# Kernel optimization log

Measured on AMD Instinct MI355X. Metric: run time of the kernel, lower is better.

## Reference

```python
import jax, jax.numpy as jnp
import numpy as np

NUM_HEADS = 8
WIN = (7, 7)


def _relative_position_index(wh, ww):
    # Same construction as the torch module (numpy, static).
    coords = np.stack(np.meshgrid(np.arange(wh), np.arange(ww), indexing='ij'))  # (2, wh, ww)
    flat = coords.reshape(2, -1)                                                 # (2, L)
    rel = flat[:, :, None] - flat[:, None, :]                                    # (2, L, L)
    rel = rel.transpose(1, 2, 0).astype(np.int64)                                # (L, L, 2)
    rel[:, :, 0] += wh - 1
    rel[:, :, 1] += ww - 1
    rel[:, :, 0] *= 2 * ww - 1
    return rel.sum(-1)  # (L, L), values in [0, (2wh-1)*(2ww-1))


def setup_inputs() -> dict:
    key = jax.random.key(0)
    k0, k1, k2, k3, k4 = jax.random.split(key, 5)
    B, C = 2048, 256
    wh, ww = WIN
    L = wh * ww
    nW = 64
    q = jax.random.normal(k0, (B, C, wh, ww), dtype=jnp.float32)
    k = jax.random.normal(k1, (B, C, wh, ww), dtype=jnp.float32)
    v = jax.random.normal(k2, (B, C, wh, ww), dtype=jnp.float32)
    # Swin-style shift mask: 0 where attend, -100 where blocked
    keep = jax.random.uniform(k3, (nW, L, L)) < 0.9
    mask = jnp.where(keep, 0.0, -100.0).astype(jnp.float32)
    n_bias = (2 * wh - 1) * (2 * ww - 1)  # 169
    rel_bias_table = 0.02 * jax.random.normal(k4, (n_bias, NUM_HEADS), dtype=jnp.float32)
    rel_pos_index = jnp.asarray(_relative_position_index(wh, ww), dtype=jnp.int32)
    return {"q": q, "k": k, "v": v, "mask": mask,
            "rel_bias_table": rel_bias_table, "rel_pos_index": rel_pos_index}


def reference(q, k, v, mask, rel_bias_table, rel_pos_index):
    b, c, wh, ww = q.shape
    L = wh * ww
    H = NUM_HEADS
    d_k = c // H
    scale = d_k ** -0.5
    qh = q.reshape(b, H, d_k, L)
    kh = k.reshape(b, H, d_k, L)
    # NOTE: the original torch code reassigns v = k.reshape(...) — values come from k.
    vh = kh
    attn = jnp.einsum('bhct,bhcs->bhts', qh, kh) * scale  # (b, H, L, L)
    bias = rel_bias_table[rel_pos_index.reshape(-1)].reshape(L, L, H)
    attn = attn + jnp.transpose(bias, (2, 0, 1))[None]    # (1, H, L, L)
    nW = mask.shape[0]
    attn = attn.reshape(b // nW, nW, H, L, L) + mask[None, :, None]
    attn = attn.reshape(b, H, L, L)
    attn = jax.nn.softmax(attn, axis=-1)
    score = jnp.einsum('bhts,bhcs->bhct', attn, vh).reshape(b, c, wh, ww)
    return (score, attn)
```

## Files before the change

### kernel.cpp

```cpp
#include <hip/hip_runtime.h>
#include <hip/hip_bf16.h>
#include <math.h>


#define LW 49
#define NH 8

typedef short s16x8 __attribute__((ext_vector_type(8)));
typedef float f32x4 __attribute__((ext_vector_type(4)));

union Frag { s16x8 v; unsigned short u[8]; };

__device__ __forceinline__ unsigned short f2bf(float x) {
    return __builtin_bit_cast(unsigned short, __float2bfloat16(x));
}
__device__ __forceinline__ float bf2f(unsigned short h) {
    return __uint_as_float(((unsigned)h) << 16);
}
__device__ __forceinline__ void split8(const float* xf, Frag& hi, Frag& lo) {
    #pragma unroll
    for (int j = 0; j < 8; j++) {
        const unsigned short hb = f2bf(xf[j]);
        hi.u[j] = hb;
        lo.u[j] = f2bf(xf[j] - bf2f(hb));
    }
}

__device__ __forceinline__ void lds_barrier() {
    asm volatile("s_waitcnt lgkmcnt(0)" ::: "memory");
    __builtin_amdgcn_s_barrier();
    asm volatile("" ::: "memory");
    __builtin_amdgcn_sched_barrier(0);
}

#define MFMA16(A, B, C) __builtin_amdgcn_mfma_f32_16x16x32_bf16((A), (B), (C), 0, 0, 0)

__global__ __launch_bounds__(256) void prep_frag_kernel(
    const float* __restrict__ mask, const float* __restrict__ table,
    const int* __restrict__ idx,
    float* __restrict__ biasF, float* __restrict__ maskF)
{
    const int i = blockIdx.x * 256 + threadIdx.x;
    const int NBF = 8 * 4096;
    const int NMF = 64 * 4096;
    if (i < NBF) {
        const int h = i >> 12, rem = i & 4095;
        const int gi = rem >> 8, lane = (rem >> 2) & 63, r = rem & 3;
        const int mt = gi >> 2, nt = gi & 3;
        const int t = mt * 16 + (lane >> 4) * 4 + r;
        const int s = nt * 16 + (lane & 15);
        biasF[i] = (t < LW && s < LW) ? table[idx[t * LW + s] * NH + h] : 0.f;
    } else if (i < NBF + NMF) {
        const int j = i - NBF;
        const int w2 = j >> 12, rem = j & 4095;
        const int gi = rem >> 8, lane = (rem >> 2) & 63, r = rem & 3;
        const int mt = gi >> 2, nt = gi & 3;
        const int t = mt * 16 + (lane >> 4) * 4 + r;
        const int s = nt * 16 + (lane & 15);
        maskF[j] = (t < LW && s < LW) ? mask[w2 * (LW * LW) + t * LW + s] : 0.f;
    }
}

__global__ __launch_bounds__(128, 4) void wa_mfma_kernel(
    const float* __restrict__ q, const float* __restrict__ k,
    const float* __restrict__ biasF, const float* __restrict__ maskF,
    float* __restrict__ score_out, float* __restrict__ attn_out)
{
    __shared__ __align__(16) unsigned short sB[6272];

    const int wv   = __builtin_amdgcn_readfirstlane((int)(threadIdx.x >> 6));
    const int bh   = blockIdx.x;
    const int h    = bh & 7;
    const int w    = (bh >> 3) & 63;
    const int lane = threadIdx.x & 63;
    const int l15  = lane & 15;
    const int g4   = lane >> 4;

    const float* qp = q + (size_t)bh * (32 * LW);
    const float* kp = k + (size_t)bh * (32 * LW);

    float k1raw[2][8], qraw[2][8], k2raw[2][8];
    #pragma unroll
    for (int ki = 0; ki < 2; ki++) {
        const int s  = (wv * 2 + ki) * 16 + l15;
        const int sc = s < LW ? s : (LW - 1);
        #pragma unroll
        for (int j = 0; j < 8; j++) k1raw[ki][j] = kp[(g4 * 8 + j) * LW + sc];
    }
    #pragma unroll
    for (int mi = 0; mi < 2; mi++) {
        const int t  = (wv * 2 + mi) * 16 + l15;
        const int tc = t < LW ? t : (LW - 1);
        #pragma unroll
        for (int j = 0; j < 8; j++) qraw[mi][j] = qp[(g4 * 8 + j) * LW + tc];
    }
    {
        const int c = wv * 16 + l15;
        #pragma unroll
        for (int ks = 0; ks < 2; ks++)
            #pragma unroll
            for (int j = 0; j < 8; j++) {
                const int s  = ks * 32 + g4 * 8 + j;
                const int sc = s < LW ? s : (LW - 1);
                k2raw[ks][j] = kp[c * LW + sc];
            }
    }

    #pragma unroll
    for (int ki = 0; ki < 2; ki++) {
        const int nt = wv * 2 + ki;
        Frag Kh, Kl;
        split8(k1raw[ki], Kh, Kl);
        *(s16x8*)&sB[nt * 512 + lane * 8]        = Kh.v;
        *(s16x8*)&sB[2048 + nt * 512 + lane * 8] = Kl.v;
    }

    Frag Qh[2], Ql[2];
    split8(qraw[0], Qh[0], Ql[0]);
    split8(qraw[1], Qh[1], Ql[1]);

    lds_barrier();

    f32x4 acc[2][4];
    #pragma unroll
    for (int mi = 0; mi < 2; mi++)
        #pragma unroll
        for (int nt = 0; nt < 4; nt++)
            #pragma unroll
            for (int r = 0; r < 4; r++) acc[mi][nt][r] = 0.f;

    #pragma unroll
    for (int nt = 0; nt < 4; nt++) {
        Frag Kh, Kl;
        Kh.v = *(const s16x8*)&sB[nt * 512 + lane * 8];
        Kl.v = *(const s16x8*)&sB[2048 + nt * 512 + lane * 8];
        #pragma unroll
        for (int mi = 0; mi < 2; mi++) {
            acc[mi][nt] = MFMA16(Qh[mi].v, Kh.v, acc[mi][nt]);
            acc[mi][nt] = MFMA16(Ql[mi].v, Kh.v, acc[mi][nt]);
            acc[mi][nt] = MFMA16(Qh[mi].v, Kl.v, acc[mi][nt]);
        }
    }

    const float scale = 0.17677669529663687f;
    const float* bF = biasF + (size_t)h * 4096 + lane * 4;
    const float* mF = maskF + (size_t)w * 4096 + lane * 4;
    #pragma unroll
    for (int mi = 0; mi < 2; mi++) {
        #pragma unroll
        for (int nt = 0; nt < 4; nt++) {
            const int gi = (wv * 2 + mi) * 4 + nt;
            const f32x4 bq = *(const f32x4*)(bF + gi * 256);
            const f32x4 mq = *(const f32x4*)(mF + gi * 256);
            const bool pad = (nt * 16 + l15) >= LW;
            #pragma unroll
            for (int r = 0; r < 4; r++) {
                const float v2 = fmaf(acc[mi][nt][r], scale, bq[r] + mq[r]);
                acc[mi][nt][r] = pad ? -1e30f : v2;
            }
        }
    }

    #pragma unroll
    for (int mi = 0; mi < 2; mi++) {
        #pragma unroll
        for (int r = 0; r < 4; r++) {
            float sm = 0.f;
            #pragma unroll
            for (int nt = 0; nt < 4; nt++) {
                const float p = __expf(acc[mi][nt][r]);
                acc[mi][nt][r] = p;
                sm += p;
            }
            sm += __shfl_xor(sm, 1);
            sm += __shfl_xor(sm, 2);
            sm += __shfl_xor(sm, 4);
            sm += __shfl_xor(sm, 8);
            const float inv = 1.0f / sm;
            #pragma unroll
            for (int nt = 0; nt < 4; nt++) acc[mi][nt][r] *= inv;
        }
    }

    lds_barrier();

    #pragma unroll
    for (int mi = 0; mi < 2; mi++) {
        #pragma unroll
        for (int r = 0; r < 4; r++) {
            const int t = (wv * 2 + mi) * 16 + g4 * 4 + r;
            if (t < LW) {
                #pragma unroll
                for (int nt = 0; nt < 4; nt++) {
                    const int s = nt * 16 + l15;
                    const float p = acc[mi][nt][r];
                    const unsigned short ph = f2bf(p);
                    const unsigned short pl = f2bf(p - bf2f(ph));
                    const unsigned idx = (unsigned)t * 64u
                        + ((((unsigned)s >> 3) ^ ((unsigned)t & 7u)) << 3)
                        + ((unsigned)s & 7u);
                    sB[idx]        = ph;
                    sB[3136 + idx] = pl;
                }
            }
        }
    }

    lds_barrier();

    float* attn_base = attn_out + (size_t)bh * (LW * LW);
    #pragma unroll
    for (int mi = 0; mi < 2; mi++) {
        #pragma unroll
        for (int r = 0; r < 4; r++) {
            const int t = (wv * 2 + mi) * 16 + g4 * 4 + r;
            if (t < LW) {
                #pragma unroll
                for (int nt = 0; nt < 4; nt++) {
                    const int s = nt * 16 + l15;
                    if (s < LW) attn_base[t * LW + s] = acc[mi][nt][r];
                }
            }
        }
    }

    Frag K2h[2], K2l[2];
    split8(k2raw[0], K2h[0], K2l[0]);
    split8(k2raw[1], K2h[1], K2l[1]);

    f32x4 acc2[4];
    #pragma unroll
    for (int nt = 0; nt < 4; nt++)
        #pragma unroll
        for (int r = 0; r < 4; r++) acc2[nt][r] = 0.f;

    #pragma unroll
    for (int ntt = 0; ntt < 4; ntt++) {
        const int t  = ntt * 16 + l15;
        const int tr = t < LW ? t : (LW - 1);
        #pragma unroll
        for (int ks = 0; ks < 2; ks++) {
            const unsigned base = (unsigned)tr * 64u
                + (((unsigned)(ks * 4 + g4) ^ ((unsigned)tr & 7u)) << 3);
            Frag Ph, Pl;
            Ph.v = *(const s16x8*)&sB[base];
            Pl.v = *(const s16x8*)&sB[3136 + base];
            acc2[ntt] = MFMA16(K2h[ks].v, Ph.v, acc2[ntt]);
            acc2[ntt] = MFMA16(K2l[ks].v, Ph.v, acc2[ntt]);
            acc2[ntt] = MFMA16(K2h[ks].v, Pl.v, acc2[ntt]);
        }
    }

    float* scp = score_out + (size_t)bh * (32 * LW);
    #pragma unroll
    for (int ntt = 0; ntt < 4; ntt++) {
        const int t = ntt * 16 + l15;
        if (t < LW) {
            #pragma unroll
            for (int r = 0; r < 4; r++) {
                const int c = wv * 16 + g4 * 4 + r;
                scp[c * LW + t] = acc2[ntt][r];
            }
        }
    }
}

__global__ __launch_bounds__(256, 4) void wa_fallback_kernel(
    const float* __restrict__ q, const float* __restrict__ k,
    const float* __restrict__ mask0, const float* __restrict__ table,
    const int* __restrict__ idx,
    float* __restrict__ score_out, float* __restrict__ attn_out)
{
    __shared__ float sPf[LW * LW];
    const int lane = threadIdx.x & 63;
    const int wv   = __builtin_amdgcn_readfirstlane((int)(threadIdx.x >> 6));
    const int bh   = blockIdx.x * 4 + wv;
    const int h    = bh & 7;
    const int w    = (bh >> 3) & 63;
    const int t    = lane;
    const int tc   = (t < LW) ? t : (LW - 1);

    const float* qp = q + (size_t)bh * (32 * LW);
    const float* kp = k + (size_t)bh * (32 * LW);

    float qreg[32];
    #pragma unroll
    for (int c = 0; c < 32; c++) qreg[c] = qp[c * LW + tc];

    float S[LW];
    #pragma unroll
    for (int s = 0; s < LW; s++) S[s] = 0.f;
    #pragma unroll
    for (int c = 0; c < 32; c++) {
        #pragma unroll
        for (int s = 0; s < LW; s++)
            S[s] = fmaf(qreg[c], kp[c * LW + s], S[s]);
    }

    const float scale = 0.17677669529663687f;
    const float* mrow = mask0 + (size_t)w * (LW * LW) + tc * LW;
    const int*   irow = idx + tc * LW;
    #pragma unroll
    for (int s = 0; s < LW; s++) {
        const float bm = table[irow[s] * NH + h] + mrow[s];
        S[s] = fmaf(S[s], scale, bm);
    }

    float m = S[0];
    #pragma unroll
    for (int s = 1; s < LW; s++) m = fmaxf(m, S[s]);
    float sum = 0.f;
    #pragma unroll
    for (int s = 0; s < LW; s++) { S[s] = __expf(S[s] - m); sum += S[s]; }
    const float invs = 1.0f / sum;
    #pragma unroll
    for (int s = 0; s < LW; s++) S[s] *= invs;

    float* attn_base = attn_out + (size_t)bh * (LW * LW);
    for (int turn = 0; turn < 4; turn++) {
        __syncthreads();
        if (turn == wv) {
            if (t < LW) {
                #pragma unroll
                for (int s = 0; s < LW; s++) sPf[t * LW + s] = S[s];
            }
            #pragma unroll
            for (int it = 0; it < 38; it++) {
                const int i = it * 64 + lane;
                if (i < LW * LW) attn_base[i] = sPf[i];
            }
        }
    }

    float* sc = score_out + (size_t)bh * (32 * LW);
    #pragma unroll
    for (int c = 0; c < 32; c++) {
        float a = 0.f;
        #pragma unroll
        for (int s = 0; s < LW; s++) a = fmaf(S[s], kp[c * LW + s], a);
        if (t < LW) sc[c * LW + t] = a;
    }
}

extern "C" void kernel_launch(void* const* d_in, const int* in_sizes, int n_in,
                              void* d_out, int out_size, void* d_ws, size_t ws_size,
                              hipStream_t stream) {
    const float* q     = (const float*)d_in[0];
    const float* k     = (const float*)d_in[1];
    const float* mask  = (const float*)d_in[3];
    const float* table = (const float*)d_in[4];
    const int*   idx   = (const int*)d_in[5];

    float* score_out = (float*)d_out;
    float* attn_out  = score_out + (size_t)2048 * 256 * 49;

    const size_t NBF = (size_t)8 * 4096;
    const size_t NMF = (size_t)64 * 4096;

    if (ws_size >= (NBF + NMF) * sizeof(float)) {
        float* biasF = (float*)d_ws;
        float* maskF = biasF + NBF;
        const int tot = (int)(NBF + NMF);
        prep_frag_kernel<<<(tot + 255) / 256, 256, 0, stream>>>(
            mask, table, idx, biasF, maskF);
        wa_mfma_kernel<<<16384, 128, 0, stream>>>(
            q, k, biasF, maskF, score_out, attn_out);
    } else {
        wa_fallback_kernel<<<4096, 256, 0, stream>>>(
            q, k, mask, table, idx, score_out, attn_out);
    }
}
```

Baseline: 502.3 us.

## Process all heads per block in a loop and fold log2e into exp2 softmax

Each block now handles one batch window and loops over all 8 heads, so the grid shrinks from 16384 to 2048 blocks and the mask pointer is computed once per block. The bias and mask fragments are pre-scaled by log2(e) in the prep kernel, and the softmax uses exp2 with a combined scale, which saves a multiply per exponential. The goal is to cut per-block launch and setup overhead. The cost is less parallelism: 2048 blocks of 2 waves on a large GPU may leave compute units underused, and the serial head loop with barriers gives less latency hiding.

```diff
diff --git a/kernel.cpp b/kernel.cpp
--- a/kernel.cpp
+++ b/kernel.cpp
@@ -43,13 +43,15 @@
     const int i = blockIdx.x * 256 + threadIdx.x;
     const int NBF = 8 * 4096;
     const int NMF = 64 * 4096;
+    const float L2E = 1.4426950408889634f;
     if (i < NBF) {
         const int h = i >> 12, rem = i & 4095;
         const int gi = rem >> 8, lane = (rem >> 2) & 63, r = rem & 3;
         const int mt = gi >> 2, nt = gi & 3;
         const int t = mt * 16 + (lane >> 4) * 4 + r;
         const int s = nt * 16 + (lane & 15);
-        biasF[i] = (t < LW && s < LW) ? table[idx[t * LW + s] * NH + h] : 0.f;
+        biasF[i] = (t < LW && s < LW) ? table[idx[t * LW + s] * NH + h] * L2E
+                                      : 0.f;
     } else if (i < NBF + NMF) {
         const int j = i - NBF;
         const int w2 = j >> 12, rem = j & 4095;
@@ -57,7 +59,8 @@
         const int mt = gi >> 2, nt = gi & 3;
         const int t = mt * 16 + (lane >> 4) * 4 + r;
         const int s = nt * 16 + (lane & 15);
-        maskF[j] = (t < LW && s < LW) ? mask[w2 * (LW * LW) + t * LW + s] : 0.f;
+        maskF[j] = (t < LW && s < LW) ? mask[w2 * (LW * LW) + t * LW + s] * L2E
+                                      : 0.f;
     }
 }
 
@@ -69,199 +72,208 @@
     __shared__ __align__(16) unsigned short sB[6272];
 
     const int wv   = __builtin_amdgcn_readfirstlane((int)(threadIdx.x >> 6));
-    const int bh   = blockIdx.x;
-    const int h    = bh & 7;
-    const int w    = (bh >> 3) & 63;
+    const int b    = blockIdx.x;
+    const int w    = b & 63;
     const int lane = threadIdx.x & 63;
     const int l15  = lane & 15;
     const int g4   = lane >> 4;
 
-    const float* qp = q + (size_t)bh * (32 * LW);
-    const float* kp = k + (size_t)bh * (32 * LW);
-
-    float k1raw[2][8], qraw[2][8], k2raw[2][8];
-    #pragma unroll
-    for (int ki = 0; ki < 2; ki++) {
-        const int s  = (wv * 2 + ki) * 16 + l15;
-        const int sc = s < LW ? s : (LW - 1);
-        #pragma unroll
-        for (int j = 0; j < 8; j++) k1raw[ki][j] = kp[(g4 * 8 + j) * LW + sc];
-    }
-    #pragma unroll
-    for (int mi = 0; mi < 2; mi++) {
-        const int t  = (wv * 2 + mi) * 16 + l15;
-        const int tc = t < LW ? t : (LW - 1);
-        #pragma unroll
-        for (int j = 0; j < 8; j++) qraw[mi][j] = qp[(g4 * 8 + j) * LW + tc];
-    }
-    {
-        const int c = wv * 16 + l15;
-        #pragma unroll
-        for (int ks = 0; ks < 2; ks++)
-            #pragma unroll
-            for (int j = 0; j < 8; j++) {
-                const int s  = ks * 32 + g4 * 8 + j;
-                const int sc = s < LW ? s : (LW - 1);
-                k2raw[ks][j] = kp[c * LW + sc];
-            }
-    }
-
-    #pragma unroll
-    for (int ki = 0; ki < 2; ki++) {
-        const int nt = wv * 2 + ki;
-        Frag Kh, Kl;
-        split8(k1raw[ki], Kh, Kl);
-        *(s16x8*)&sB[nt * 512 + lane * 8]        = Kh.v;
-        *(s16x8*)&sB[2048 + nt * 512 + lane * 8] = Kl.v;
-    }
-
-    Frag Qh[2], Ql[2];
-    split8(qraw[0], Qh[0], Ql[0]);
-    split8(qraw[1], Qh[1], Ql[1]);
-
-    lds_barrier();
-
-    f32x4 acc[2][4];
-    #pragma unroll
-    for (int mi = 0; mi < 2; mi++)
+    const float scale2 = 0.17677669529663687f * 1.4426950408889634f;
+    const float* mF = maskF + (size_t)w * 4096 + lane * 4;
+
+    #pragma unroll 1
+    for (int h = 0; h < NH; h++) {
+        const int bh = b * NH + h;
+        const float* qp = q + (size_t)bh * (32 * LW);
+        const float* kp = k + (size_t)bh * (32 * LW);
+
+        float k1raw[2][8], qraw[2][8], k2raw[2][8];
+        #pragma unroll
+        for (int ki = 0; ki < 2; ki++) {
+            const int s  = (wv * 2 + ki) * 16 + l15;
+            const int sc = s < LW ? s : (LW - 1);
+            #pragma unroll
+            for (int j = 0; j < 8; j++)
+                k1raw[ki][j] = kp[(g4 * 8 + j) * LW + sc];
+        }
+        #pragma unroll
+        for (int mi = 0; mi < 2; mi++) {
+            const int t  = (wv * 2 + mi) * 16 + l15;
+            const int tc = t < LW ? t : (LW - 1);
+            #pragma unroll
+            for (int j = 0; j < 8; j++)
+                qraw[mi][j] = qp[(g4 * 8 + j) * LW + tc];
+        }
+        {
+            const int c = wv * 16 + l15;
+            #pragma unroll
+            for (int ks = 0; ks < 2; ks++)
+                #pragma unroll
+                for (int j = 0; j < 8; j++) {
+                    const int s  = ks * 32 + g4 * 8 + j;
+                    const int sc = s < LW ? s : (LW - 1);
+                    k2raw[ks][j] = kp[c * LW + sc];
+                }
+        }
+
+        #pragma unroll
+        for (int ki = 0; ki < 2; ki++) {
+            const int nt = wv * 2 + ki;
+            Frag Kh, Kl;
+            split8(k1raw[ki], Kh, Kl);
+            *(s16x8*)&sB[nt * 512 + lane * 8]        = Kh.v;
+            *(s16x8*)&sB[2048 + nt * 512 + lane * 8] = Kl.v;
+        }
+
+        Frag Qh[2], Ql[2];
+        split8(qraw[0], Qh[0], Ql[0]);
+        split8(qraw[1], Qh[1], Ql[1]);
+
+        lds_barrier();
+
+        f32x4 acc[2][4];
+        #pragma unroll
+        for (int mi = 0; mi < 2; mi++)
+            #pragma unroll
+            for (int nt = 0; nt < 4; nt++)
+                #pragma unroll
+                for (int r = 0; r < 4; r++) acc[mi][nt][r] = 0.f;
+
+        #pragma unroll
+        for (int nt = 0; nt < 4; nt++) {
+            Frag Kh, Kl;
+            Kh.v = *(const s16x8*)&sB[nt * 512 + lane * 8];
+            Kl.v = *(const s16x8*)&sB[2048 + nt * 512 + lane * 8];
+            #pragma unroll
+            for (int mi = 0; mi < 2; mi++) {
+                acc[mi][nt] = MFMA16(Qh[mi].v, Kh.v, acc[mi][nt]);
+                acc[mi][nt] = MFMA16(Ql[mi].v, Kh.v, acc[mi][nt]);
+                acc[mi][nt] = MFMA16(Qh[mi].v, Kl.v, acc[mi][nt]);
+            }
+        }
+
+        const float* bF = biasF + (size_t)h * 4096 + lane * 4;
+        #pragma unroll
+        for (int mi = 0; mi < 2; mi++) {
+            #pragma unroll
+            for (int nt = 0; nt < 4; nt++) {
+                const int gi = (wv * 2 + mi) * 4 + nt;
+                const f32x4 bq = *(const f32x4*)(bF + gi * 256);
+                const f32x4 mq = *(const f32x4*)(mF + gi * 256);
+                const bool pad = (nt * 16 + l15) >= LW;
+                #pragma unroll
+                for (int r = 0; r < 4; r++) {
+                    const float v2 = fmaf(acc[mi][nt][r], scale2,
+                                          bq[r] + mq[r]);
+                    acc[mi][nt][r] = pad ? -1e30f : v2;
+                }
+            }
+        }
+
+        #pragma unroll
+        for (int mi = 0; mi < 2; mi++) {
+            #pragma unroll
+            for (int r = 0; r < 4; r++) {
+                float sm = 0.f;
+                #pragma unroll
+                for (int nt = 0; nt < 4; nt++) {
+                    const float p = __builtin_exp2f(acc[mi][nt][r]);
+                    acc[mi][nt][r] = p;
+                    sm += p;
+                }
+                sm += __shfl_xor(sm, 1);
+                sm += __shfl_xor(sm, 2);
+                sm += __shfl_xor(sm, 4);
+                sm += __shfl_xor(sm, 8);
+                const float inv = 1.0f / sm;
+                #pragma unroll
+                for (int nt = 0; nt < 4; nt++) acc[mi][nt][r] *= inv;
+            }
+        }
+
+        lds_barrier();
+
+        #pragma unroll
+        for (int mi = 0; mi < 2; mi++) {
+            #pragma unroll
+            for (int r = 0; r < 4; r++) {
+                const int t = (wv * 2 + mi) * 16 + g4 * 4 + r;
+                if (t < LW) {
+                    #pragma unroll
+                    for (int nt = 0; nt < 4; nt++) {
+                        const int s = nt * 16 + l15;
+                        const float p = acc[mi][nt][r];
+                        const unsigned short ph = f2bf(p);
+                        const unsigned short pl = f2bf(p - bf2f(ph));
+                        const unsigned idx = (unsigned)t * 64u
+                            + ((((unsigned)s >> 3) ^ ((unsigned)t & 7u)) << 3)
+                            + ((unsigned)s & 7u);
+                        sB[idx]        = ph;
+                        sB[3136 + idx] = pl;
+                    }
+                }
+            }
+        }
+
+        lds_barrier();
+
+        float* attn_base = attn_out + (size_t)bh * (LW * LW);
+        #pragma unroll
+        for (int mi = 0; mi < 2; mi++) {
+            #pragma unroll
+            for (int r = 0; r < 4; r++) {
+                const int t = (wv * 2 + mi) * 16 + g4 * 4 + r;
+                if (t < LW) {
+                    #pragma unroll
+                    for (int nt = 0; nt < 4; nt++) {
+                        const int s = nt * 16 + l15;
+                        if (s < LW) attn_base[t * LW + s] = acc[mi][nt][r];
+                    }
+                }
+            }
+        }
+
+        Frag K2h[2], K2l[2];
+        split8(k2raw[0], K2h[0], K2l[0]);
+        split8(k2raw[1], K2h[1], K2l[1]);
+
+        f32x4 acc2[4];
         #pragma unroll
         for (int nt = 0; nt < 4; nt++)
             #pragma unroll
-            for (int r = 0; r < 4; r++) acc[mi][nt][r] = 0.f;
-
-    #pragma unroll
-    for (int nt = 0; nt < 4; nt++) {
-        Frag Kh, Kl;
-        Kh.v = *(const s16x8*)&sB[nt * 512 + lane * 8];
-        Kl.v = *(const s16x8*)&sB[2048 + nt * 512 + lane * 8];
-        #pragma unroll
-        for (int mi = 0; mi < 2; mi++) {
-            acc[mi][nt] = MFMA16(Qh[mi].v, Kh.v, acc[mi][nt]);
-            acc[mi][nt] = MFMA16(Ql[mi].v, Kh.v, acc[mi][nt]);
-            acc[mi][nt] = MFMA16(Qh[mi].v, Kl.v, acc[mi][nt]);
-        }
-    }
-
-    const float scale = 0.17677669529663687f;
-    const float* bF = biasF + (size_t)h * 4096 + lane * 4;
-    const float* mF = maskF + (size_t)w * 4096 + lane * 4;
-    #pragma unroll
-    for (int mi = 0; mi < 2; mi++) {
-        #pragma unroll
-        for (int nt = 0; nt < 4; nt++) {
-            const int gi = (wv * 2 + mi) * 4 + nt;
-            const f32x4 bq = *(const f32x4*)(bF + gi * 256);
-            const f32x4 mq = *(const f32x4*)(mF + gi * 256);
-            const bool pad = (nt * 16 + l15) >= LW;
-            #pragma unroll
-            for (int r = 0; r < 4; r++) {
-                const float v2 = fmaf(acc[mi][nt][r], scale, bq[r] + mq[r]);
-                acc[mi][nt][r] = pad ? -1e30f : v2;
-            }
-        }
-    }
-
-    #pragma unroll
-    for (int mi = 0; mi < 2; mi++) {
-        #pragma unroll
-        for (int r = 0; r < 4; r++) {
-            float sm = 0.f;
-            #pragma unroll
-            for (int nt = 0; nt < 4; nt++) {
-                const float p = __expf(acc[mi][nt][r]);
-                acc[mi][nt][r] = p;
-                sm += p;
-            }
-            sm += __shfl_xor(sm, 1);
-            sm += __shfl_xor(sm, 2);
-            sm += __shfl_xor(sm, 4);
-            sm += __shfl_xor(sm, 8);
-            const float inv = 1.0f / sm;
-            #pragma unroll
-            for (int nt = 0; nt < 4; nt++) acc[mi][nt][r] *= inv;
-        }
-    }
-
-    lds_barrier();
-
-    #pragma unroll
-    for (int mi = 0; mi < 2; mi++) {
-        #pragma unroll
-        for (int r = 0; r < 4; r++) {
-            const int t = (wv * 2 + mi) * 16 + g4 * 4 + r;
+            for (int r = 0; r < 4; r++) acc2[nt][r] = 0.f;
+
+        #pragma unroll
+        for (int ntt = 0; ntt < 4; ntt++) {
+            const int t  = ntt * 16 + l15;
+            const int tr = t < LW ? t : (LW - 1);
+            #pragma unroll
+            for (int ks = 0; ks < 2; ks++) {
+                const unsigned base = (unsigned)tr * 64u
+                    + (((unsigned)(ks * 4 + g4) ^ ((unsigned)tr & 7u)) << 3);
+                Frag Ph, Pl;
+                Ph.v = *(const s16x8*)&sB[base];
+                Pl.v = *(const s16x8*)&sB[3136 + base];
+                acc2[ntt] = MFMA16(K2h[ks].v, Ph.v, acc2[ntt]);
+                acc2[ntt] = MFMA16(K2l[ks].v, Ph.v, acc2[ntt]);
+                acc2[ntt] = MFMA16(K2h[ks].v, Pl.v, acc2[ntt]);
+            }
+        }
+
+        float* scp = score_out + (size_t)bh * (32 * LW);
+        #pragma unroll
+        for (int ntt = 0; ntt < 4; ntt++) {
+            const int t = ntt * 16 + l15;
             if (t < LW) {
                 #pragma unroll
-                for (int nt = 0; nt < 4; nt++) {
-                    const int s = nt * 16 + l15;
-                    const float p = acc[mi][nt][r];
-                    const unsigned short ph = f2bf(p);
-                    const unsigned short pl = f2bf(p - bf2f(ph));
-                    const unsigned idx = (unsigned)t * 64u
-                        + ((((unsigned)s >> 3) ^ ((unsigned)t & 7u)) << 3)
-                        + ((unsigned)s & 7u);
-                    sB[idx]        = ph;
-                    sB[3136 + idx] = pl;
-                }
-            }
-        }
-    }
-
-    lds_barrier();
-
-    float* attn_base = attn_out + (size_t)bh * (LW * LW);
-    #pragma unroll
-    for (int mi = 0; mi < 2; mi++) {
-        #pragma unroll
-        for (int r = 0; r < 4; r++) {
-            const int t = (wv * 2 + mi) * 16 + g4 * 4 + r;
-            if (t < LW) {
-                #pragma unroll
-                for (int nt = 0; nt < 4; nt++) {
-                    const int s = nt * 16 + l15;
-                    if (s < LW) attn_base[t * LW + s] = acc[mi][nt][r];
-                }
-            }
-        }
-    }
-
-    Frag K2h[2], K2l[2];
-    split8(k2raw[0], K2h[0], K2l[0]);
-    split8(k2raw[1], K2h[1], K2l[1]);
-
-    f32x4 acc2[4];
-    #pragma unroll
-    for (int nt = 0; nt < 4; nt++)
-        #pragma unroll
-        for (int r = 0; r < 4; r++) acc2[nt][r] = 0.f;
-
-    #pragma unroll
-    for (int ntt = 0; ntt < 4; ntt++) {
-        const int t  = ntt * 16 + l15;
-        const int tr = t < LW ? t : (LW - 1);
-        #pragma unroll
-        for (int ks = 0; ks < 2; ks++) {
-            const unsigned base = (unsigned)tr * 64u
-                + (((unsigned)(ks * 4 + g4) ^ ((unsigned)tr & 7u)) << 3);
-            Frag Ph, Pl;
-            Ph.v = *(const s16x8*)&sB[base];
-            Pl.v = *(const s16x8*)&sB[3136 + base];
-            acc2[ntt] = MFMA16(K2h[ks].v, Ph.v, acc2[ntt]);
-            acc2[ntt] = MFMA16(K2l[ks].v, Ph.v, acc2[ntt]);
-            acc2[ntt] = MFMA16(K2h[ks].v, Pl.v, acc2[ntt]);
-        }
-    }
-
-    float* scp = score_out + (size_t)bh * (32 * LW);
-    #pragma unroll
-    for (int ntt = 0; ntt < 4; ntt++) {
-        const int t = ntt * 16 + l15;
-        if (t < LW) {
-            #pragma unroll
-            for (int r = 0; r < 4; r++) {
-                const int c = wv * 16 + g4 * 4 + r;
-                scp[c * LW + t] = acc2[ntt][r];
-            }
-        }
+                for (int r = 0; r < 4; r++) {
+                    const int c = wv * 16 + g4 * 4 + r;
+                    scp[c * LW + t] = acc2[ntt][r];
+                }
+            }
+        }
+
+        lds_barrier();
     }
 }
 
@@ -363,7 +375,7 @@
         const int tot = (int)(NBF + NMF);
         prep_frag_kernel<<<(tot + 255) / 256, 256, 0, stream>>>(
             mask, table, idx, biasF, maskF);
-        wa_mfma_kernel<<<16384, 128, 0, stream>>>(
+        wa_mfma_kernel<<<2048, 128, 0, stream>>>(
             q, k, biasF, maskF, score_out, attn_out);
     } else {
         wa_fallback_kernel<<<4096, 256, 0, stream>>>(
```

New measurement: 670.0 us. 1.33x slower.
